# Optimization experiments

Measured on AMD Instinct MI355X. Metric: run time of the kernel, lower is better.

## Reference

```python
import jax, jax.numpy as jnp
import numpy as np

DIM = 1024
N_HEADS = 16
N_KV = 4
HEAD_DIM = 64
FFN = 4096
EPS = 1e-6
B, S = 2, 2048
ROPE_BASE = 10000.0


def rmsnorm(x, w, eps=EPS):
    ms = jnp.mean(jnp.square(x), axis=-1, keepdims=True)
    return x * jax.lax.rsqrt(ms + eps) * w


def apply_rotary(x, cos, sin):
    # x: [B,H,S,hd]; cos/sin: [S, hd//2] -> broadcast over B,H
    half = x.shape[-1] // 2
    x1, x2 = x[..., :half], x[..., half:]
    c = cos[None, None, :, :]
    s = sin[None, None, :, :]
    return jnp.concatenate((x1 * c + x2 * s, x2 * c - x1 * s), axis=-1)


def setup_inputs() -> dict:
    key = jax.random.key(0)
    ks = jax.random.split(key, 10)
    w = lambda k, shp: jax.random.normal(k, shp, dtype=jnp.float32) * 0.02
    pos = jnp.arange(S, dtype=jnp.float32)
    inv_freq = 1.0 / (ROPE_BASE ** (jnp.arange(0, HEAD_DIM // 2, dtype=jnp.float32) / (HEAD_DIM // 2)))
    ang = pos[:, None] * inv_freq[None, :]
    return {
        "x": jax.random.normal(ks[0], (B, S, DIM), dtype=jnp.float32),
        "w_norm1": jnp.ones((DIM,), jnp.float32),
        "wq": w(ks[1], (DIM, N_HEADS * HEAD_DIM)),
        "wk": w(ks[2], (DIM, N_KV * HEAD_DIM)),
        "wv": w(ks[3], (DIM, N_KV * HEAD_DIM)),
        "wo": w(ks[4], (N_HEADS * HEAD_DIM, DIM)),
        "attn_scale": jnp.ones((DIM,), jnp.float32),
        "w_norm2": jnp.ones((DIM,), jnp.float32),
        "wg": w(ks[5], (DIM, FFN)),
        "wu": w(ks[6], (DIM, FFN)),
        "wd": w(ks[7], (FFN, DIM)),
        "mlp_scale": jnp.ones((DIM,), jnp.float32),
        "cos": jnp.cos(ang),
        "sin": jnp.sin(ang),
    }


def block_forward(x, w_norm1, wq, wk, wv, wo, attn_scale, w_norm2, wg, wu, wd, mlp_scale, cos, sin):
    b, s, d = x.shape
    # ---- attention sub-block (pre-norm, RoPE, causal GQA SDPA, scaled residual) ----
    xn = rmsnorm(x, w_norm1)
    q = (xn @ wq).reshape(b, s, N_HEADS, HEAD_DIM).transpose(0, 2, 1, 3)  # [B,H,S,hd]
    k = (xn @ wk).reshape(b, s, N_KV, HEAD_DIM).transpose(0, 2, 1, 3)    # [B,KV,S,hd]
    v = (xn @ wv).reshape(b, s, N_KV, HEAD_DIM).transpose(0, 2, 1, 3)
    q = apply_rotary(q, cos, sin)
    k = apply_rotary(k, cos, sin)
    rep = N_HEADS // N_KV
    k = jnp.repeat(k, rep, axis=1)  # GQA expand -> [B,H,S,hd]
    v = jnp.repeat(v, rep, axis=1)
    scale = 1.0 / np.sqrt(HEAD_DIM)
    scores = jnp.einsum("bhqd,bhkd->bhqk", q, k) * scale
    causal = jnp.tril(jnp.ones((s, s), dtype=bool))
    scores = jnp.where(causal[None, None], scores, jnp.finfo(scores.dtype).min)
    probs = jax.nn.softmax(scores, axis=-1)
    attn = jnp.einsum("bhqk,bhkd->bhqd", probs, v)
    attn = attn.transpose(0, 2, 1, 3).reshape(b, s, N_HEADS * HEAD_DIM)
    x = x + (attn @ wo) * attn_scale[None, None, :]
    # ---- MLP sub-block (pre-norm, fused gate/up SwiGLU, down proj, scaled residual) ----
    xn2 = rmsnorm(x, w_norm2)
    hidden = jax.nn.silu(xn2 @ wg) * (xn2 @ wu)  # SwiGLU
    x = x + (hidden @ wd) * mlp_scale[None, None, :]
    return x


def reference(x, w_norm1, wq, wk, wv, wo, attn_scale, w_norm2, wg, wu, wd, mlp_scale, cos, sin):
    return block_forward(x, w_norm1, wq, wk, wv, wo, attn_scale, w_norm2, wg, wu, wd, mlp_scale, cos, sin)
```

## Files before the change

kernel.cpp:

```cpp
#include <hip/hip_runtime.h>
#include <hip/hip_bf16.h>
#include <cstdint>

typedef unsigned short u16;
typedef unsigned int u32;
typedef __attribute__((ext_vector_type(4))) float f32x4;
typedef __attribute__((ext_vector_type(8))) __bf16 bf16x8;

#define NH 16
#define NKV 4
#define SEQ 2048
#define NTOK 4096

__device__ inline u16 f2bf(float f) {
  return __builtin_bit_cast(u16, __float2bfloat16(f));
}
__device__ inline float bf2f(u16 u) {
  return __bfloat162float(__builtin_bit_cast(__hip_bfloat16, u));
}

#define GLDS(gp, lp) __builtin_amdgcn_global_load_lds( \
    (__attribute__((address_space(1))) void*)(gp), \
    (__attribute__((address_space(3))) void*)(lp), 16, 0, 0)

#define VMCNT0 asm volatile("s_waitcnt vmcnt(0)" ::: "memory")

__global__ __launch_bounds__(256) void rmsnorm_kernel(
    const float* __restrict__ x, const float* __restrict__ w,
    u16* __restrict__ out) {
  int row = blockIdx.x;
  int tid = threadIdx.x;
  const float4 v = reinterpret_cast<const float4*>(x + (size_t)row * 1024)[tid];
  float ss = v.x * v.x + v.y * v.y + v.z * v.z + v.w * v.w;
#pragma unroll
  for (int off = 32; off; off >>= 1) ss += __shfl_xor(ss, off);
  __shared__ float red[4];
  int lane = tid & 63, wid = tid >> 6;
  if (lane == 0) red[wid] = ss;
  __syncthreads();
  float tot = red[0] + red[1] + red[2] + red[3];
  float r = rsqrtf(tot * (1.0f / 1024.0f) + 1e-6f);
  const float4 wv = reinterpret_cast<const float4*>(w)[tid];
  ushort4 o;
  o.x = f2bf(v.x * r * wv.x);
  o.y = f2bf(v.y * r * wv.y);
  o.z = f2bf(v.z * r * wv.z);
  o.w = f2bf(v.w * r * wv.w);
  reinterpret_cast<ushort4*>(out + (size_t)row * 1024)[tid] = o;
}

__global__ __launch_bounds__(256) void transpose_cast_kernel(
    const float* __restrict__ src, u16* __restrict__ dst, int K, int N) {
  __shared__ float tile[32][33];
  int n0 = blockIdx.x * 32, k0 = blockIdx.y * 32;
  int tx = threadIdx.x & 31, ty = threadIdx.x >> 5;
#pragma unroll
  for (int i = 0; i < 4; i++)
    tile[ty + i * 8][tx] = src[(size_t)(k0 + ty + i * 8) * N + n0 + tx];
  __syncthreads();
#pragma unroll
  for (int i = 0; i < 4; i++)
    dst[(size_t)(n0 + ty + i * 8) * K + k0 + tx] = f2bf(tile[tx][ty + i * 8]);
}

template <int EP>
__device__ inline void epi_store(float v, size_t idx, int col,
                                 float* __restrict__ outf,
                                 const float* __restrict__ res,
                                 const float* __restrict__ scale,
                                 u16* __restrict__ outb) {
  if (EP == 0) {
    outf[idx] = v;
  } else if (EP == 1) {
    outf[idx] = res[idx] + v * scale[col];
  } else if (EP == 2) {
    outb[idx] = f2bf(v / (1.0f + __expf(-v)));
  } else {
    outb[idx] = f2bf(bf2f(outb[idx]) * v);
  }
}

template <int EP>
__global__ __launch_bounds__(256, 1) void gemmB(
    const u16* __restrict__ A, const u16* __restrict__ Bt,
    int M, int N, int K,
    float* __restrict__ outf, const float* __restrict__ res,
    const float* __restrict__ scale, u16* __restrict__ outb) {
  __shared__ u16 SA[2][128 * 64];
  __shared__ u16 SB[2][128 * 64];
  const int tid = threadIdx.x, lane = tid & 63, w = tid >> 6;
  const int wr = w >> 1, wc = w & 1;
  const int lg = lane >> 4, lc = lane & 15, cx = lc & 7;

  const int r8 = blockIdx.x & 7, j = blockIdx.x >> 3;
  const int bm = ((r8 << 2) + (j & 3)) << 7;
  const int bn = (j >> 2) << 7;

  const int swrow = lane >> 3;
  const int swcol = (lane & 7) ^ swrow;
  const u16* gA = A + (size_t)(bm + w * 32 + swrow) * K + swcol * 8;
  const u16* gB = Bt + (size_t)(bn + w * 32 + swrow) * K + swcol * 8;

  const int NT = K >> 6;
  f32x4 acc[4][4] = {};

#define SG2(T_) do { int sl_ = (T_) & 1; size_t ko_ = (size_t)(T_) * 64; \
    GLDS(gA + ko_,                   &SA[sl_][(w * 32) * 64]); \
    GLDS(gA + ko_ + (size_t)8 * K,   &SA[sl_][(w * 32 + 8) * 64]); \
    GLDS(gA + ko_ + (size_t)16 * K,  &SA[sl_][(w * 32 + 16) * 64]); \
    GLDS(gA + ko_ + (size_t)24 * K,  &SA[sl_][(w * 32 + 24) * 64]); \
    GLDS(gB + ko_,                   &SB[sl_][(w * 32) * 64]); \
    GLDS(gB + ko_ + (size_t)8 * K,   &SB[sl_][(w * 32 + 8) * 64]); \
    GLDS(gB + ko_ + (size_t)16 * K,  &SB[sl_][(w * 32 + 16) * 64]); \
    GLDS(gB + ko_ + (size_t)24 * K,  &SB[sl_][(w * 32 + 24) * 64]); } while (0)

  SG2(0);
  VMCNT0;
  __builtin_amdgcn_s_barrier();

  for (int t = 0; t < NT; ++t) {
    const u16* sa = &SA[t & 1][0];
    const u16* sb = &SB[t & 1][0];
    const bool more = (t + 1 < NT);

    bf16x8 bfr[4][2], afr[4][2];
#pragma unroll
    for (int n = 0; n < 4; n++) {
      const int row = wc * 64 + n * 16 + lc;
#pragma unroll
      for (int ks = 0; ks < 2; ks++)
        bfr[n][ks] = *reinterpret_cast<const bf16x8*>(
            &sb[row * 64 + ((((ks << 2) | lg) ^ cx) << 3)]);
    }
#pragma unroll
    for (int i = 0; i < 4; i++) {
      const int row = wr * 64 + i * 16 + lc;
#pragma unroll
      for (int ks = 0; ks < 2; ks++)
        afr[i][ks] = *reinterpret_cast<const bf16x8*>(
            &sa[row * 64 + ((((ks << 2) | lg) ^ cx) << 3)]);
    }
    if (more) SG2(t + 1);
    __builtin_amdgcn_s_setprio(1);
#pragma unroll
    for (int i = 0; i < 4; i++)
#pragma unroll
      for (int n = 0; n < 4; n++) {
        acc[i][n] = __builtin_amdgcn_mfma_f32_16x16x32_bf16(afr[i][0], bfr[n][0], acc[i][n], 0, 0, 0);
        acc[i][n] = __builtin_amdgcn_mfma_f32_16x16x32_bf16(afr[i][1], bfr[n][1], acc[i][n], 0, 0, 0);
      }
    __builtin_amdgcn_s_setprio(0);
    VMCNT0;
    __builtin_amdgcn_s_barrier();
  }
#undef SG2

#pragma unroll
  for (int mi = 0; mi < 4; mi++)
#pragma unroll
    for (int ni = 0; ni < 4; ni++)
#pragma unroll
      for (int rg = 0; rg < 4; rg++) {
        const int row = bm + wr * 64 + mi * 16 + lg * 4 + rg;
        const int col = bn + wc * 64 + ni * 16 + lc;
        epi_store<EP>(acc[mi][ni][rg], (size_t)row * N + col, col, outf, res, scale, outb);
      }
}

__global__ __launch_bounds__(512, 2) void gateup_kernel(
    const u16* __restrict__ A, const u16* __restrict__ Bg,
    const u16* __restrict__ Bu, u16* __restrict__ outb) {
  const int K = 1024, N = 4096;
  __shared__ u16 SA[2][256 * 32];
  __shared__ u16 SG[2][128 * 32];
  __shared__ u16 SU[2][128 * 32];
  const int tid = threadIdx.x, lane = tid & 63, w = tid >> 6;
  const int wr = w >> 1, wc = w & 1;
  const int lg = lane >> 4, lc = lane & 15;

  const int r8 = blockIdx.x & 7, j = blockIdx.x >> 3;
  const int bm = (((r8 >> 1) << 2) + (j & 3)) << 8;
  const int bn = ((r8 & 1) * 16 + (j >> 2)) << 7;

  const int srow = tid >> 2;
  const int scs = ((tid & 3) ^ (srow & 3)) * 8;
  const u16* gAs = A + (size_t)(bm + srow) * K + scs;
  const u16* gGs = Bg + (size_t)(bn + srow) * K + scs;
  const u16* gUs = Bu + (size_t)(bn + srow) * K + scs;

  f32x4 accG[4][4] = {}, accU[4][4] = {};

#define SGU(T_) do { int sl_ = (T_) & 1; size_t ko_ = (size_t)(T_) * 32; \
    GLDS(gAs + ko_,                   &SA[sl_][w * 512]); \
    GLDS(gAs + ko_ + (size_t)128 * K, &SA[sl_][4096 + w * 512]); \
    GLDS(gGs + ko_,                   &SG[sl_][w * 512]); \
    GLDS(gUs + ko_,                   &SU[sl_][w * 512]); } while (0)

  SGU(0);
  VMCNT0;
  __builtin_amdgcn_s_barrier();

  for (int t = 0; t < 32; ++t) {
    const u16* sa = &SA[t & 1][0];
    const u16* sg = &SG[t & 1][0];
    const u16* su = &SU[t & 1][0];
    const bool more = (t + 1 < 32);

    bf16x8 afr[4], gfr[4], ufr[4];
#pragma unroll
    for (int i = 0; i < 4; i++) {
      const int row = wr * 64 + i * 16 + lc;
      afr[i] = *reinterpret_cast<const bf16x8*>(
          &sa[row * 32 + ((lg ^ (lc & 3)) << 3)]);
    }
#pragma unroll
    for (int n = 0; n < 4; n++) {
      const int row = wc * 64 + n * 16 + lc;
      const int off = row * 32 + ((lg ^ (lc & 3)) << 3);
      gfr[n] = *reinterpret_cast<const bf16x8*>(&sg[off]);
      ufr[n] = *reinterpret_cast<const bf16x8*>(&su[off]);
    }
    if (more) SGU(t + 1);
    __builtin_amdgcn_s_setprio(1);
#pragma unroll
    for (int i = 0; i < 4; i++)
#pragma unroll
      for (int n = 0; n < 4; n++) {
        accG[i][n] = __builtin_amdgcn_mfma_f32_16x16x32_bf16(afr[i], gfr[n], accG[i][n], 0, 0, 0);
        accU[i][n] = __builtin_amdgcn_mfma_f32_16x16x32_bf16(afr[i], ufr[n], accU[i][n], 0, 0, 0);
      }
    __builtin_amdgcn_s_setprio(0);
    VMCNT0;
    __builtin_amdgcn_s_barrier();
  }
#undef SGU

#pragma unroll
  for (int mi = 0; mi < 4; mi++)
#pragma unroll
    for (int ni = 0; ni < 4; ni++)
#pragma unroll
      for (int rg = 0; rg < 4; rg++) {
        const int row = bm + wr * 64 + mi * 16 + lg * 4 + rg;
        const int col = bn + wc * 64 + ni * 16 + lc;
        const float g = accG[mi][ni][rg];
        const float u = accU[mi][ni][rg];
        outb[(size_t)row * N + col] = f2bf((g / (1.0f + __expf(-g))) * u);
      }
}

__global__ __launch_bounds__(256) void rope_kernel(
    const float* __restrict__ qkv, const float* __restrict__ cosb,
    const float* __restrict__ sinb, u16* __restrict__ qr, u16* __restrict__ kr) {
  int idx = blockIdx.x * 256 + threadIdx.x;
  int d = idx & 31;
  int t = idx >> 5;
  int head = t % 20;
  int bs = t / 20;
  int s = bs & (SEQ - 1);
  int b = bs >> 11;
  const float* row = qkv + (size_t)bs * 1536;
  float c = cosb[s * 32 + d], sn = sinb[s * 32 + d];
  const float QSC = 0.18033688011112042f;
  float x1, x2;
  if (head < 16) {
    x1 = row[head * 64 + d];
    x2 = row[head * 64 + d + 32];
    size_t o = ((size_t)(b * NH + head) * SEQ + s) * 64 + d;
    qr[o] = f2bf((x1 * c + x2 * sn) * QSC);
    qr[o + 32] = f2bf((x2 * c - x1 * sn) * QSC);
  } else {
    int kh = head - 16;
    x1 = row[1024 + kh * 64 + d];
    x2 = row[1024 + kh * 64 + d + 32];
    size_t o = ((size_t)(b * NKV + kh) * SEQ + s) * 64 + d;
    kr[o] = f2bf(x1 * c + x2 * sn);
    kr[o + 32] = f2bf(x2 * c - x1 * sn);
  }
}

__global__ __launch_bounds__(256) void vtrans_kernel(
    const float* __restrict__ qkv, u16* __restrict__ vt) {
  int blk = blockIdx.x;
  int st = blk & 31; blk >>= 5;
  int kvh = blk & 3; blk >>= 2;
  int b = blk;
  __shared__ u16 tile[64][65];
  int tx = threadIdx.x & 63;
  int ty = threadIdx.x >> 6;
  int s0 = st * 64;
#pragma unroll
  for (int i = 0; i < 16; i++) {
    int sl = i * 4 + ty;
    tile[sl][tx] = f2bf(qkv[(size_t)(b * SEQ + s0 + sl) * 1536 + 1280 + kvh * 64 + tx]);
  }
  __syncthreads();
  size_t vbase = (size_t)(b * NKV + kvh) * 64 * SEQ;
#pragma unroll
  for (int i = 0; i < 16; i++) {
    int dd = i * 4 + ty;
    vt[vbase + (size_t)dd * SEQ + s0 + tx] = tile[tx][dd];
  }
}

__global__ __launch_bounds__(512, 1) void attn_kernel(
    const u16* __restrict__ qr, const u16* __restrict__ kr,
    const u16* __restrict__ vt, u16* __restrict__ out) {
  __shared__ u16 Ks[2][64 * 64];
  __shared__ u16 Vs[2][64 * 64];
  __shared__ u16 Ps[8][32 * 64];

  const int n = blockIdx.x;
  const int g = n & 7;
  const int b = g >> 2, kvh = g & 3;
  const int h = kvh * 4 + ((n >> 3) & 3);
  const int j = n >> 5;

  const int tid = threadIdx.x;
  const int lane = tid & 63, w = tid >> 6;
  const int lg = lane >> 4, lc = lane & 15;
  const int lc7 = lc & 7;

  const int isH = (w ^ (w >> 2)) & 1;
  const int strip = isH ? (15 - j) : j;
  const int q0w = strip * 128 + (w >> 1) * 32;
  const int nt = 2 * (15 - j) + 2;

  bf16x8 qf[2][2];
  {
    const u16* qp = qr + ((size_t)(b * NH + h) * SEQ + q0w + lc) * 64 + lg * 8;
#pragma unroll
    for (int qt = 0; qt < 2; qt++) {
      qf[qt][0] = *reinterpret_cast<const bf16x8*>(qp + qt * 16 * 64);
      qf[qt][1] = *reinterpret_cast<const bf16x8*>(qp + qt * 16 * 64 + 32);
    }
  }
  VMCNT0;

  const int srow = lane >> 3;
  const int scw = ((lane & 7) ^ srow) << 3;
  const u16* ksrc = kr + (size_t)(b * NKV + kvh) * SEQ * 64 + (size_t)(w * 8 + srow) * 64 + scw;
  const u16* vsrc = vt + ((size_t)(b * NKV + kvh) * 64 + w * 8 + srow) * SEQ + scw;
  u16* Pw = &Ps[w][0];

#define STAGEA(bufi, t) do { \
    GLDS(ksrc + (size_t)(t) * 64 * 64, &Ks[bufi][(w * 8) * 64]); \
    GLDS(vsrc + (size_t)(t) * 64,      &Vs[bufi][(w * 8) * 64]); \
  } while (0)

  STAGEA(0, 0);

  float mm[2] = {-1e30f, -1e30f}, ll[2] = {0.0f, 0.0f};
  f32x4 oacc[2][4] = {};

  int buf = 0;
  for (int t = 0; t < nt; ++t) {
    if (t + 1 < nt) {
      STAGEA(buf ^ 1, t + 1);
      asm volatile("s_waitcnt vmcnt(2)" ::: "memory");
    } else {
      VMCNT0;
    }
    __builtin_amdgcn_s_barrier();
    __builtin_amdgcn_sched_barrier(0);

    const int c0 = t * 64;
    if (c0 <= q0w + 31) {
      bf16x8 kf[4][2];
#pragma unroll
      for (int ni = 0; ni < 4; ni++) {
        const int row = ni * 16 + lc;
#pragma unroll
        for (int hf = 0; hf < 2; hf++)
          kf[ni][hf] = *reinterpret_cast<const bf16x8*>(
              &Ks[buf][row * 64 + ((((hf * 64 + lg * 16)) ^ (lc7 << 4)) >> 1)]);
      }
      f32x4 sc[4][2] = {};
      __builtin_amdgcn_s_setprio(1);
#pragma unroll
      for (int ni = 0; ni < 4; ni++)
#pragma unroll
        for (int qt = 0; qt < 2; qt++) {
          sc[ni][qt] = __builtin_amdgcn_mfma_f32_16x16x32_bf16(kf[ni][0], qf[qt][0], sc[ni][qt], 0, 0, 0);
          sc[ni][qt] = __builtin_amdgcn_mfma_f32_16x16x32_bf16(kf[ni][1], qf[qt][1], sc[ni][qt], 0, 0, 0);
        }
      __builtin_amdgcn_s_setprio(0);
      bf16x8 vf[4][2];
#pragma unroll
      for (int dt = 0; dt < 4; dt++) {
        const int row = dt * 16 + lc;
#pragma unroll
        for (int ks = 0; ks < 2; ks++)
          vf[dt][ks] = *reinterpret_cast<const bf16x8*>(
              &Vs[buf][row * 64 + (((ks * 64 + lg * 16) ^ (lc7 << 4)) >> 1)]);
      }
      if (c0 + 63 > q0w) {
#pragma unroll
        for (int qt = 0; qt < 2; qt++) {
          const int q = q0w + qt * 16 + lc;
#pragma unroll
          for (int ni = 0; ni < 4; ni++)
#pragma unroll
            for (int rg = 0; rg < 4; rg++)
              if (c0 + ni * 16 + lg * 4 + rg > q) sc[ni][qt][rg] = -1e30f;
        }
      }
      float mx[2];
#pragma unroll
      for (int qt = 0; qt < 2; qt++) {
        float v = -1e30f;
#pragma unroll
        for (int ni = 0; ni < 4; ni++)
#pragma unroll
          for (int rg = 0; rg < 4; rg++) v = fmaxf(v, sc[ni][qt][rg]);
        v = fmaxf(v, __shfl_xor(v, 16));
        v = fmaxf(v, __shfl_xor(v, 32));
        mx[qt] = v;
      }
      if (!__all(mx[0] - mm[0] <= 11.5f && mx[1] - mm[1] <= 11.5f)) {
        float al[2];
#pragma unroll
        for (int qt = 0; qt < 2; qt++) {
          float mn = fmaxf(mm[qt], mx[qt]);
          al[qt] = exp2f(mm[qt] - mn);
          mm[qt] = mn;
          ll[qt] *= al[qt];
        }
#pragma unroll
        for (int qt = 0; qt < 2; qt++)
#pragma unroll
          for (int rg = 0; rg < 4; rg++) {
            float a = __shfl(al[qt], lg * 4 + rg);
#pragma unroll
            for (int dt = 0; dt < 4; dt++) oacc[qt][dt][rg] *= a;
          }
      }
#pragma unroll
      for (int qt = 0; qt < 2; qt++) {
        float rs = 0.0f;
#pragma unroll
        for (int ni = 0; ni < 4; ni++)
#pragma unroll
          for (int rg = 0; rg < 4; rg++) {
            float p = exp2f(sc[ni][qt][rg] - mm[qt]);
            sc[ni][qt][rg] = p;
            rs += p;
          }
        rs += __shfl_xor(rs, 16);
        rs += __shfl_xor(rs, 32);
        ll[qt] += rs;
      }
#pragma unroll
      for (int qt = 0; qt < 2; qt++)
#pragma unroll
        for (int ni = 0; ni < 4; ni++) {
          ushort4 pk;
          pk.x = f2bf(sc[ni][qt][0]);
          pk.y = f2bf(sc[ni][qt][1]);
          pk.z = f2bf(sc[ni][qt][2]);
          pk.w = f2bf(sc[ni][qt][3]);
          *reinterpret_cast<ushort4*>(
              &Pw[(qt * 16 + lc) * 64 + (((ni * 32 + lg * 8) ^ (lc7 << 4)) >> 1)]) = pk;
        }
      __builtin_amdgcn_s_setprio(1);
#pragma unroll
      for (int qt = 0; qt < 2; qt++)
#pragma unroll
        for (int ks = 0; ks < 2; ks++) {
          bf16x8 pa = *reinterpret_cast<const bf16x8*>(
              &Pw[(qt * 16 + lc) * 64 + (((ks * 64 + lg * 16) ^ (lc7 << 4)) >> 1)]);
#pragma unroll
          for (int dt = 0; dt < 4; dt++)
            oacc[qt][dt] = __builtin_amdgcn_mfma_f32_16x16x32_bf16(pa, vf[dt][ks], oacc[qt][dt], 0, 0, 0);
        }
      __builtin_amdgcn_s_setprio(0);
    }
    asm volatile("s_waitcnt lgkmcnt(0)" ::: "memory");
    __builtin_amdgcn_s_barrier();
    __builtin_amdgcn_sched_barrier(0);
    buf ^= 1;
  }
#undef STAGEA

#pragma unroll
  for (int qt = 0; qt < 2; qt++) {
    const float li = 1.0f / ll[qt];
#pragma unroll
    for (int rg = 0; rg < 4; rg++) {
      float liq = __shfl(li, lg * 4 + rg);
      int q = q0w + qt * 16 + lg * 4 + rg;
      u16* orow = out + (size_t)(b * SEQ + q) * 1024 + h * 64 + lc;
#pragma unroll
      for (int dt = 0; dt < 4; dt++)
        orow[dt * 16] = f2bf(oacc[qt][dt][rg] * liq);
    }
  }
}

extern "C" void kernel_launch(void* const* d_in, const int* in_sizes, int n_in,
                              void* d_out, int out_size, void* d_ws, size_t ws_size,
                              hipStream_t stream) {
  const float* x = (const float*)d_in[0];
  const float* w_norm1 = (const float*)d_in[1];
  const float* wq = (const float*)d_in[2];
  const float* wk = (const float*)d_in[3];
  const float* wv = (const float*)d_in[4];
  const float* wo = (const float*)d_in[5];
  const float* attn_scale = (const float*)d_in[6];
  const float* w_norm2 = (const float*)d_in[7];
  const float* wg = (const float*)d_in[8];
  const float* wu = (const float*)d_in[9];
  const float* wd = (const float*)d_in[10];
  const float* mlp_scale = (const float*)d_in[11];
  const float* cosb = (const float*)d_in[12];
  const float* sinb = (const float*)d_in[13];
  float* out = (float*)d_out;

  char* ws = (char*)d_ws;
  u16* wqkv_t = (u16*)(ws + 0);
  u16* wo_t = (u16*)(ws + 3145728);
  u16* wg_t = (u16*)(ws + 5242880);
  u16* wu_t = (u16*)(ws + 13631488);
  u16* wd_t = (u16*)(ws + 22020096);
  u16* xn = (u16*)(ws + 30408704);
  float* qkv = (float*)(ws + 38797312);
  u16* attn_o = (u16*)(ws + 38797312);
  float* x1 = (float*)(ws + 47185920);
  u16* q_rope = (u16*)(ws + 63963136);
  u16* k_rope = (u16*)(ws + 72351744);
  u16* vt = (u16*)(ws + 74448896);
  u16* hbuf = (u16*)(ws + 63963136);

  dim3 tb(256);
  transpose_cast_kernel<<<dim3(32, 32), tb, 0, stream>>>(wq, wqkv_t, 1024, 1024);
  transpose_cast_kernel<<<dim3(8, 32), tb, 0, stream>>>(wk, wqkv_t + (size_t)1024 * 1024, 1024, 256);
  transpose_cast_kernel<<<dim3(8, 32), tb, 0, stream>>>(wv, wqkv_t + (size_t)1280 * 1024, 1024, 256);
  transpose_cast_kernel<<<dim3(32, 32), tb, 0, stream>>>(wo, wo_t, 1024, 1024);
  transpose_cast_kernel<<<dim3(128, 32), tb, 0, stream>>>(wg, wg_t, 1024, 4096);
  transpose_cast_kernel<<<dim3(128, 32), tb, 0, stream>>>(wu, wu_t, 1024, 4096);
  transpose_cast_kernel<<<dim3(32, 128), tb, 0, stream>>>(wd, wd_t, 4096, 1024);

  rmsnorm_kernel<<<4096, tb, 0, stream>>>(x, w_norm1, xn);
  gemmB<0><<<dim3(384), dim3(256), 0, stream>>>(xn, wqkv_t, 4096, 1536, 1024, qkv, nullptr, nullptr, nullptr);
  rope_kernel<<<10240, tb, 0, stream>>>(qkv, cosb, sinb, q_rope, k_rope);
  vtrans_kernel<<<2 * 4 * 32, tb, 0, stream>>>(qkv, vt);
  attn_kernel<<<256, dim3(512), 0, stream>>>(q_rope, k_rope, vt, attn_o);
  gemmB<1><<<dim3(256), dim3(256), 0, stream>>>(attn_o, wo_t, 4096, 1024, 1024, x1, x, attn_scale, nullptr);
  rmsnorm_kernel<<<4096, tb, 0, stream>>>(x1, w_norm2, xn);
  gateup_kernel<<<dim3(512), dim3(512), 0, stream>>>(xn, wg_t, wu_t, hbuf);
  gemmB<1><<<dim3(256), dim3(256), 0, stream>>>(hbuf, wd_t, 4096, 1024, 4096, out, x1, mlp_scale, nullptr);
}
```

Baseline: 266.7 us.

## Retile gate/up GEMM to 128x128 tiles with BK=64 and 1024 blocks

Result: no change. 269.8 us (+1.2%).

```diff
diff --git a/kernel.cpp b/kernel.cpp
--- a/kernel.cpp
+++ b/kernel.cpp
@@ -167,68 +167,77 @@
       }
 }
 
-__global__ __launch_bounds__(512, 2) void gateup_kernel(
+__global__ __launch_bounds__(512, 1) void gateup_kernel(
     const u16* __restrict__ A, const u16* __restrict__ Bg,
     const u16* __restrict__ Bu, u16* __restrict__ outb) {
   const int K = 1024, N = 4096;
-  __shared__ u16 SA[2][256 * 32];
-  __shared__ u16 SG[2][128 * 32];
-  __shared__ u16 SU[2][128 * 32];
+  __shared__ u16 SA[2][128 * 64];
+  __shared__ u16 SG[2][128 * 64];
+  __shared__ u16 SU[2][128 * 64];
   const int tid = threadIdx.x, lane = tid & 63, w = tid >> 6;
-  const int wr = w >> 1, wc = w & 1;
-  const int lg = lane >> 4, lc = lane & 15;
+  const int wr = w >> 2, wc = w & 3;
+  const int lg = lane >> 4, lc = lane & 15, cx = lc & 7;
 
   const int r8 = blockIdx.x & 7, j = blockIdx.x >> 3;
-  const int bm = (((r8 >> 1) << 2) + (j & 3)) << 8;
-  const int bn = ((r8 & 1) * 16 + (j >> 2)) << 7;
-
-  const int srow = tid >> 2;
-  const int scs = ((tid & 3) ^ (srow & 3)) * 8;
-  const u16* gAs = A + (size_t)(bm + srow) * K + scs;
-  const u16* gGs = Bg + (size_t)(bn + srow) * K + scs;
-  const u16* gUs = Bu + (size_t)(bn + srow) * K + scs;
-
-  f32x4 accG[4][4] = {}, accU[4][4] = {};
-
-#define SGU(T_) do { int sl_ = (T_) & 1; size_t ko_ = (size_t)(T_) * 32; \
-    GLDS(gAs + ko_,                   &SA[sl_][w * 512]); \
-    GLDS(gAs + ko_ + (size_t)128 * K, &SA[sl_][4096 + w * 512]); \
-    GLDS(gGs + ko_,                   &SG[sl_][w * 512]); \
-    GLDS(gUs + ko_,                   &SU[sl_][w * 512]); } while (0)
+  const int bm = ((r8 >> 1) * 8 + (j & 7)) << 7;
+  const int bn = ((r8 & 1) * 16 + (j >> 3)) << 7;
+
+  const int swrow = lane >> 3;
+  const int swcol = (lane & 7) ^ swrow;
+  const u16* gAs = A + (size_t)(bm + w * 16 + swrow) * K + swcol * 8;
+  const u16* gGs = Bg + (size_t)(bn + w * 16 + swrow) * K + swcol * 8;
+  const u16* gUs = Bu + (size_t)(bn + w * 16 + swrow) * K + swcol * 8;
+
+  f32x4 accG[4][2] = {}, accU[4][2] = {};
+
+#define SGU(T_) do { int sl_ = (T_) & 1; size_t ko_ = (size_t)(T_) * 64; \
+    GLDS(gAs + ko_,                  &SA[sl_][(w * 16) * 64]); \
+    GLDS(gAs + ko_ + (size_t)8 * K,  &SA[sl_][(w * 16 + 8) * 64]); \
+    GLDS(gGs + ko_,                  &SG[sl_][(w * 16) * 64]); \
+    GLDS(gGs + ko_ + (size_t)8 * K,  &SG[sl_][(w * 16 + 8) * 64]); \
+    GLDS(gUs + ko_,                  &SU[sl_][(w * 16) * 64]); \
+    GLDS(gUs + ko_ + (size_t)8 * K,  &SU[sl_][(w * 16 + 8) * 64]); } while (0)
 
   SGU(0);
   VMCNT0;
   __builtin_amdgcn_s_barrier();
 
-  for (int t = 0; t < 32; ++t) {
+  for (int t = 0; t < 16; ++t) {
     const u16* sa = &SA[t & 1][0];
     const u16* sg = &SG[t & 1][0];
     const u16* su = &SU[t & 1][0];
-    const bool more = (t + 1 < 32);
-
-    bf16x8 afr[4], gfr[4], ufr[4];
+    const bool more = (t + 1 < 16);
+
+    bf16x8 afr[4][2], gfr[2][2], ufr[2][2];
 #pragma unroll
     for (int i = 0; i < 4; i++) {
       const int row = wr * 64 + i * 16 + lc;
-      afr[i] = *reinterpret_cast<const bf16x8*>(
-          &sa[row * 32 + ((lg ^ (lc & 3)) << 3)]);
-    }
-#pragma unroll
-    for (int n = 0; n < 4; n++) {
-      const int row = wc * 64 + n * 16 + lc;
-      const int off = row * 32 + ((lg ^ (lc & 3)) << 3);
-      gfr[n] = *reinterpret_cast<const bf16x8*>(&sg[off]);
-      ufr[n] = *reinterpret_cast<const bf16x8*>(&su[off]);
+#pragma unroll
+      for (int ks = 0; ks < 2; ks++)
+        afr[i][ks] = *reinterpret_cast<const bf16x8*>(
+            &sa[row * 64 + ((((ks << 2) | lg) ^ cx) << 3)]);
+    }
+#pragma unroll
+    for (int n = 0; n < 2; n++) {
+      const int row = wc * 32 + n * 16 + lc;
+#pragma unroll
+      for (int ks = 0; ks < 2; ks++) {
+        const int off = row * 64 + ((((ks << 2) | lg) ^ cx) << 3);
+        gfr[n][ks] = *reinterpret_cast<const bf16x8*>(&sg[off]);
+        ufr[n][ks] = *reinterpret_cast<const bf16x8*>(&su[off]);
+      }
     }
     if (more) SGU(t + 1);
     __builtin_amdgcn_s_setprio(1);
 #pragma unroll
     for (int i = 0; i < 4; i++)
 #pragma unroll
-      for (int n = 0; n < 4; n++) {
-        accG[i][n] = __builtin_amdgcn_mfma_f32_16x16x32_bf16(afr[i], gfr[n], accG[i][n], 0, 0, 0);
-        accU[i][n] = __builtin_amdgcn_mfma_f32_16x16x32_bf16(afr[i], ufr[n], accU[i][n], 0, 0, 0);
-      }
+      for (int n = 0; n < 2; n++)
+#pragma unroll
+        for (int ks = 0; ks < 2; ks++) {
+          accG[i][n] = __builtin_amdgcn_mfma_f32_16x16x32_bf16(afr[i][ks], gfr[n][ks], accG[i][n], 0, 0, 0);
+          accU[i][n] = __builtin_amdgcn_mfma_f32_16x16x32_bf16(afr[i][ks], ufr[n][ks], accU[i][n], 0, 0, 0);
+        }
     __builtin_amdgcn_s_setprio(0);
     VMCNT0;
     __builtin_amdgcn_s_barrier();
@@ -238,11 +247,11 @@
 #pragma unroll
   for (int mi = 0; mi < 4; mi++)
 #pragma unroll
-    for (int ni = 0; ni < 4; ni++)
+    for (int ni = 0; ni < 2; ni++)
 #pragma unroll
       for (int rg = 0; rg < 4; rg++) {
         const int row = bm + wr * 64 + mi * 16 + lg * 4 + rg;
-        const int col = bn + wc * 64 + ni * 16 + lc;
+        const int col = bn + wc * 32 + ni * 16 + lc;
         const float g = accG[mi][ni][rg];
         const float u = accU[mi][ni][rg];
         outb[(size_t)row * N + col] = f2bf((g / (1.0f + __expf(-g))) * u);
@@ -547,6 +556,6 @@
   attn_kernel<<<256, dim3(512), 0, stream>>>(q_rope, k_rope, vt, attn_o);
   gemmB<1><<<dim3(256), dim3(256), 0, stream>>>(attn_o, wo_t, 4096, 1024, 1024, x1, x, attn_scale, nullptr);
   rmsnorm_kernel<<<4096, tb, 0, stream>>>(x1, w_norm2, xn);
-  gateup_kernel<<<dim3(512), dim3(512), 0, stream>>>(xn, wg_t, wu_t, hbuf);
+  gateup_kernel<<<dim3(1024), dim3(512), 0, stream>>>(xn, wg_t, wu_t, hbuf);
   gemmB<1><<<dim3(256), dim3(256), 0, stream>>>(hbuf, wd_t, 4096, 1024, 4096, out, x1, mlp_scale, nullptr);
 }
```

## Fuse RoPE and V transpose into the QKV projection GEMM epilogue

Applied to the files above, without the earlier changes.

New measurement: 267.2 us, median of 2. No clear change (+0.2%).

```diff
diff --git a/kernel.cpp b/kernel.cpp
--- a/kernel.cpp
+++ b/kernel.cpp
@@ -167,6 +167,129 @@
       }
 }
 
+__global__ __launch_bounds__(256, 1) void qkvrope_kernel(
+    const u16* __restrict__ A, const u16* __restrict__ Bt,
+    const float* __restrict__ cosb, const float* __restrict__ sinb,
+    u16* __restrict__ qr, u16* __restrict__ kr, u16* __restrict__ vt) {
+  const int N = 1536, K = 1024, NT = 16;
+  __shared__ u16 SA[2][128 * 64];
+  __shared__ u16 SB[2][128 * 64];
+  __shared__ u16 TT[4][64 * 66];
+  const int tid = threadIdx.x, lane = tid & 63, w = tid >> 6;
+  const int wr = w >> 1, wc = w & 1;
+  const int lg = lane >> 4, lc = lane & 15, cx = lc & 7;
+
+  const int r8 = blockIdx.x & 7, j = blockIdx.x >> 3;
+  const int bm = ((r8 << 2) + (j & 3)) << 7;
+  const int bn = (j >> 2) << 7;
+
+  const int swrow = lane >> 3;
+  const int swcol = (lane & 7) ^ swrow;
+  const u16* gA = A + (size_t)(bm + w * 32 + swrow) * K + swcol * 8;
+  const u16* gB = Bt + (size_t)(bn + w * 32 + swrow) * K + swcol * 8;
+
+  f32x4 acc[4][4] = {};
+
+#define SG2(T_) do { int sl_ = (T_) & 1; size_t ko_ = (size_t)(T_) * 64; \
+    GLDS(gA + ko_,                   &SA[sl_][(w * 32) * 64]); \
+    GLDS(gA + ko_ + (size_t)8 * K,   &SA[sl_][(w * 32 + 8) * 64]); \
+    GLDS(gA + ko_ + (size_t)16 * K,  &SA[sl_][(w * 32 + 16) * 64]); \
+    GLDS(gA + ko_ + (size_t)24 * K,  &SA[sl_][(w * 32 + 24) * 64]); \
+    GLDS(gB + ko_,                   &SB[sl_][(w * 32) * 64]); \
+    GLDS(gB + ko_ + (size_t)8 * K,   &SB[sl_][(w * 32 + 8) * 64]); \
+    GLDS(gB + ko_ + (size_t)16 * K,  &SB[sl_][(w * 32 + 16) * 64]); \
+    GLDS(gB + ko_ + (size_t)24 * K,  &SB[sl_][(w * 32 + 24) * 64]); } while (0)
+
+  SG2(0);
+  VMCNT0;
+  __builtin_amdgcn_s_barrier();
+
+  for (int t = 0; t < NT; ++t) {
+    const u16* sa = &SA[t & 1][0];
+    const u16* sb = &SB[t & 1][0];
+    const bool more = (t + 1 < NT);
+
+    bf16x8 bfr[4][2], afr[4][2];
+#pragma unroll
+    for (int n = 0; n < 4; n++) {
+      const int row = wc * 64 + n * 16 + lc;
+#pragma unroll
+      for (int ks = 0; ks < 2; ks++)
+        bfr[n][ks] = *reinterpret_cast<const bf16x8*>(
+            &sb[row * 64 + ((((ks << 2) | lg) ^ cx) << 3)]);
+    }
+#pragma unroll
+    for (int i = 0; i < 4; i++) {
+      const int row = wr * 64 + i * 16 + lc;
+#pragma unroll
+      for (int ks = 0; ks < 2; ks++)
+        afr[i][ks] = *reinterpret_cast<const bf16x8*>(
+            &sa[row * 64 + ((((ks << 2) | lg) ^ cx) << 3)]);
+    }
+    if (more) SG2(t + 1);
+    __builtin_amdgcn_s_setprio(1);
+#pragma unroll
+    for (int i = 0; i < 4; i++)
+#pragma unroll
+      for (int n = 0; n < 4; n++) {
+        acc[i][n] = __builtin_amdgcn_mfma_f32_16x16x32_bf16(afr[i][0], bfr[n][0], acc[i][n], 0, 0, 0);
+        acc[i][n] = __builtin_amdgcn_mfma_f32_16x16x32_bf16(afr[i][1], bfr[n][1], acc[i][n], 0, 0, 0);
+      }
+    __builtin_amdgcn_s_setprio(0);
+    VMCNT0;
+    __builtin_amdgcn_s_barrier();
+  }
+#undef SG2
+
+  const int colbase = bn + wc * 64;
+  const int hh = colbase >> 6;
+  const float QSC = 0.18033688011112042f;
+
+  if (hh < 20) {
+    const bool isQ = (hh < 16);
+    const int head = isQ ? hh : hh - 16;
+    u16* dst = isQ ? qr : kr;
+    const int hstride = isQ ? NH : NKV;
+    const float scq = isQ ? QSC : 1.0f;
+#pragma unroll
+    for (int mi = 0; mi < 4; mi++)
+#pragma unroll
+      for (int rg = 0; rg < 4; rg++) {
+        const int row = bm + wr * 64 + mi * 16 + lg * 4 + rg;
+        const int s = row & (SEQ - 1), b = row >> 11;
+        u16* obase = dst + ((size_t)(b * hstride + head) * SEQ + s) * 64;
+#pragma unroll
+        for (int ni = 0; ni < 2; ni++) {
+          const int d = ni * 16 + lc;
+          const float c = cosb[s * 32 + d];
+          const float sn = sinb[s * 32 + d];
+          const float x1 = acc[mi][ni][rg];
+          const float x2 = acc[mi][ni + 2][rg];
+          obase[d] = f2bf((x1 * c + x2 * sn) * scq);
+          obase[d + 32] = f2bf((x2 * c - x1 * sn) * scq);
+        }
+      }
+  } else {
+    const int kv = hh - 20;
+    u16* tw = &TT[w][0];
+#pragma unroll
+    for (int mi = 0; mi < 4; mi++)
+#pragma unroll
+      for (int ni = 0; ni < 4; ni++)
+#pragma unroll
+        for (int rg = 0; rg < 4; rg++)
+          tw[(ni * 16 + lc) * 66 + mi * 16 + lg * 4 + rg] = f2bf(acc[mi][ni][rg]);
+    asm volatile("s_waitcnt lgkmcnt(0)" ::: "memory");
+    __builtin_amdgcn_sched_barrier(0);
+    const int r0 = bm + wr * 64;
+    const int s0 = r0 & (SEQ - 1), b = r0 >> 11;
+    u16* vbase = vt + (size_t)(b * NKV + kv) * 64 * SEQ + s0 + lane;
+#pragma unroll 4
+    for (int dd = 0; dd < 64; dd++)
+      vbase[(size_t)dd * SEQ] = tw[dd * 66 + lane];
+  }
+}
+
 __global__ __launch_bounds__(512, 2) void gateup_kernel(
     const u16* __restrict__ A, const u16* __restrict__ Bg,
     const u16* __restrict__ Bu, u16* __restrict__ outb) {
@@ -247,60 +370,6 @@
         const float u = accU[mi][ni][rg];
         outb[(size_t)row * N + col] = f2bf((g / (1.0f + __expf(-g))) * u);
       }
-}
-
-__global__ __launch_bounds__(256) void rope_kernel(
-    const float* __restrict__ qkv, const float* __restrict__ cosb,
-    const float* __restrict__ sinb, u16* __restrict__ qr, u16* __restrict__ kr) {
-  int idx = blockIdx.x * 256 + threadIdx.x;
-  int d = idx & 31;
-  int t = idx >> 5;
-  int head = t % 20;
-  int bs = t / 20;
-  int s = bs & (SEQ - 1);
-  int b = bs >> 11;
-  const float* row = qkv + (size_t)bs * 1536;
-  float c = cosb[s * 32 + d], sn = sinb[s * 32 + d];
-  const float QSC = 0.18033688011112042f;
-  float x1, x2;
-  if (head < 16) {
-    x1 = row[head * 64 + d];
-    x2 = row[head * 64 + d + 32];
-    size_t o = ((size_t)(b * NH + head) * SEQ + s) * 64 + d;
-    qr[o] = f2bf((x1 * c + x2 * sn) * QSC);
-    qr[o + 32] = f2bf((x2 * c - x1 * sn) * QSC);
-  } else {
-    int kh = head - 16;
-    x1 = row[1024 + kh * 64 + d];
-    x2 = row[1024 + kh * 64 + d + 32];
-    size_t o = ((size_t)(b * NKV + kh) * SEQ + s) * 64 + d;
-    kr[o] = f2bf(x1 * c + x2 * sn);
-    kr[o + 32] = f2bf(x2 * c - x1 * sn);
-  }
-}
-
-__global__ __launch_bounds__(256) void vtrans_kernel(
-    const float* __restrict__ qkv, u16* __restrict__ vt) {
-  int blk = blockIdx.x;
-  int st = blk & 31; blk >>= 5;
-  int kvh = blk & 3; blk >>= 2;
-  int b = blk;
-  __shared__ u16 tile[64][65];
-  int tx = threadIdx.x & 63;
-  int ty = threadIdx.x >> 6;
-  int s0 = st * 64;
-#pragma unroll
-  for (int i = 0; i < 16; i++) {
-    int sl = i * 4 + ty;
-    tile[sl][tx] = f2bf(qkv[(size_t)(b * SEQ + s0 + sl) * 1536 + 1280 + kvh * 64 + tx]);
-  }
-  __syncthreads();
-  size_t vbase = (size_t)(b * NKV + kvh) * 64 * SEQ;
-#pragma unroll
-  for (int i = 0; i < 16; i++) {
-    int dd = i * 4 + ty;
-    vt[vbase + (size_t)dd * SEQ + s0 + tx] = tile[tx][dd];
-  }
 }
 
 __global__ __launch_bounds__(512, 1) void attn_kernel(
@@ -523,7 +592,6 @@
   u16* wu_t = (u16*)(ws + 13631488);
   u16* wd_t = (u16*)(ws + 22020096);
   u16* xn = (u16*)(ws + 30408704);
-  float* qkv = (float*)(ws + 38797312);
   u16* attn_o = (u16*)(ws + 38797312);
   float* x1 = (float*)(ws + 47185920);
   u16* q_rope = (u16*)(ws + 63963136);
@@ -541,12 +609,10 @@
   transpose_cast_kernel<<<dim3(32, 128), tb, 0, stream>>>(wd, wd_t, 4096, 1024);
 
   rmsnorm_kernel<<<4096, tb, 0, stream>>>(x, w_norm1, xn);
-  gemmB<0><<<dim3(384), dim3(256), 0, stream>>>(xn, wqkv_t, 4096, 1536, 1024, qkv, nullptr, nullptr, nullptr);
-  rope_kernel<<<10240, tb, 0, stream>>>(qkv, cosb, sinb, q_rope, k_rope);
-  vtrans_kernel<<<2 * 4 * 32, tb, 0, stream>>>(qkv, vt);
+  qkvrope_kernel<<<dim3(384), tb, 0, stream>>>(xn, wqkv_t, cosb, sinb, q_rope, k_rope, vt);
   attn_kernel<<<256, dim3(512), 0, stream>>>(q_rope, k_rope, vt, attn_o);
-  gemmB<1><<<dim3(256), dim3(256), 0, stream>>>(attn_o, wo_t, 4096, 1024, 1024, x1, x, attn_scale, nullptr);
+  gemmB<1><<<dim3(256), tb, 0, stream>>>(attn_o, wo_t, 4096, 1024, 1024, x1, x, attn_scale, nullptr);
   rmsnorm_kernel<<<4096, tb, 0, stream>>>(x1, w_norm2, xn);
   gateup_kernel<<<dim3(512), dim3(512), 0, stream>>>(xn, wg_t, wu_t, hbuf);
-  gemmB<1><<<dim3(256), dim3(256), 0, stream>>>(hbuf, wd_t, 4096, 1024, 4096, out, x1, mlp_scale, nullptr);
-}
+  gemmB<1><<<dim3(256), tb, 0, stream>>>(hbuf, wd_t, 4096, 1024, 4096, out, x1, mlp_scale, nullptr);
+}
```
